# Kernel tuning notes

Hardware: AMD Instinct MI355X
Metric: run time of the kernel (lower is better)

## Reference

```python
import jax, jax.numpy as jnp
import numpy as np

T, D = 4096, 1536          # tokens, hidden
H, KV, HD = 24, 8, 64      # heads, kv heads, head dim
E, TOPK, F = 32, 8, 512    # experts, top-k, expert intermediate
FS = 1024                  # shared-MLP intermediate
THETA = 10000.0
AMULT = 0.015625           # attention_multiplier (replaces 1/sqrt(hd))
RMULT = 0.22               # residual_multiplier
EPS = 1e-6


def setup_inputs() -> dict:
    key = jax.random.key(0)
    ks = jax.random.split(key, 12)
    s = 0.02
    return {
        'positions': jnp.arange(T, dtype=jnp.int32),
        'hidden_states': jax.random.normal(ks[0], (T, D), jnp.float32),
        'ln1_w': jnp.ones((D,), jnp.float32),
        'wq': jax.random.normal(ks[1], (D, H * HD), jnp.float32) * s,
        'wk': jax.random.normal(ks[2], (D, KV * HD), jnp.float32) * s,
        'wv': jax.random.normal(ks[3], (D, KV * HD), jnp.float32) * s,
        'wo': jax.random.normal(ks[4], (H * HD, D), jnp.float32) * s,
        'ln2_w': jnp.ones((D,), jnp.float32),
        'router_w': jax.random.normal(ks[5], (D, E), jnp.float32) * s,
        'w_gate_up': jax.random.normal(ks[6], (E, D, 2 * F), jnp.float32) * s,
        'w_down': jax.random.normal(ks[7], (E, F, D), jnp.float32) * s,
        'shared_gate_up': jax.random.normal(ks[8], (D, 2 * FS), jnp.float32) * s,
        'shared_down': jax.random.normal(ks[9], (FS, D), jnp.float32) * s,
    }


def _rmsnorm(x, w):
    var = jnp.mean(x * x, axis=-1, keepdims=True)
    return x * jax.lax.rsqrt(var + EPS) * w


def _rope(x, positions):
    # x: [T, nH, HD], neox-style half rotation
    half = HD // 2
    inv_freq = 1.0 / (THETA ** (jnp.arange(half, dtype=jnp.float32) / half))
    ang = positions.astype(jnp.float32)[:, None] * inv_freq[None, :]  # [T, half]
    cos, sin = jnp.cos(ang)[:, None, :], jnp.sin(ang)[:, None, :]
    x1, x2 = x[..., :half], x[..., half:]
    return jnp.concatenate([x1 * cos - x2 * sin, x2 * cos + x1 * sin], axis=-1)


def _silu_and_mul(gu):
    g, u = jnp.split(gu, 2, axis=-1)
    return jax.nn.silu(g) * u


def reference(positions, hidden_states, ln1_w, wq, wk, wv, wo, ln2_w,
              router_w, w_gate_up, w_down, shared_gate_up, shared_down):
    # ---- attention block ----
    residual = hidden_states
    h = _rmsnorm(hidden_states, ln1_w)
    q = _rope((h @ wq).reshape(T, H, HD), positions)
    k = _rope((h @ wk).reshape(T, KV, HD), positions)
    v = (h @ wv).reshape(T, KV, HD)
    k = jnp.repeat(k, H // KV, axis=1)  # GQA expand -> [T, H, HD]
    v = jnp.repeat(v, H // KV, axis=1)
    scores = jnp.einsum('thd,shd->hts', q, k) * AMULT
    mask = jnp.tril(jnp.ones((T, T), dtype=bool))
    scores = jnp.where(mask[None], scores, jnp.finfo(scores.dtype).min)
    probs = jax.nn.softmax(scores, axis=-1)
    attn = jnp.einsum('hts,shd->thd', probs, v).reshape(T, H * HD) @ wo
    hidden = residual + attn * RMULT

    # ---- MoE + shared MLP block ----
    residual = hidden
    h = _rmsnorm(hidden, ln2_w)
    # router: top-k logits, softmax over selected (renormalized gates)
    logits = h @ router_w                          # [T, E]
    topv, topi = jax.lax.top_k(logits, TOPK)       # [T, TOPK]
    gates = jax.nn.softmax(topv, axis=-1)
    # per-token dense expert weight map [T, E] (zero for unselected experts)
    wmap = jnp.sum(jax.nn.one_hot(topi, E, dtype=h.dtype) * gates[..., None], axis=1)
    gu = jnp.einsum('td,edf->tef', h, w_gate_up)   # [T, E, 2F]
    act = _silu_and_mul(gu)                        # [T, E, F]
    moe_out = jnp.einsum('tef,efd,te->td', act, w_down, wmap)
    # shared SiLU MLP
    shared = _silu_and_mul(h @ shared_gate_up) @ shared_down
    hidden = residual + (moe_out + shared) * RMULT
    return hidden
```

## Files before the change

kernel.cpp:

```cpp
#include <hip/hip_runtime.h>
#include <stdint.h>

using u16 = unsigned short;
using u32 = unsigned int;

typedef __attribute__((ext_vector_type(8))) short short8;
typedef __attribute__((ext_vector_type(4))) short short4v;
typedef __attribute__((ext_vector_type(4))) float f32x4;

#define MFMA16(a,b,c) __builtin_amdgcn_mfma_f32_16x16x32_bf16(a,b,c,0,0,0)
#define QSCL 0.022542110325192448f


__device__ __forceinline__ u16 f2bf(float f){
  u32 u = __float_as_uint(f);
  u += 0x7fffu + ((u>>16)&1u);
  return (u16)(u>>16);
}
__device__ __forceinline__ float bf2f(u16 b){ return __uint_as_float(((u32)b)<<16); }

__device__ __forceinline__ void gload16(const void* g, void* l){
  __builtin_amdgcn_global_load_lds(
      (const __attribute__((address_space(1))) u32*)g,
      (__attribute__((address_space(3))) u32*)l, 16, 0, 0);
}

template<int CTRL>
__device__ __forceinline__ float dppf(float x){
  return __int_as_float(__builtin_amdgcn_mov_dpp(__float_as_int(x), CTRL, 0xf, 0xf, true));
}
__device__ __forceinline__ float red16_sum(float x){
  x += dppf<0x128>(x);
  x += dppf<0x124>(x);
  x += dppf<0x122>(x);
  x += dppf<0x121>(x);
  return x;
}

__global__ __launch_bounds__(256) void k_wt(const float* __restrict__ src,
    u16* __restrict__ dst, int K, int N, long sstride, long dstride)
{
  __shared__ float tile[64][65];
  int nb = blockIdx.x*64, kb = blockIdx.y*64;
  const float* S = src + (long)blockIdx.z*sstride;
  u16* D = dst + (long)blockIdx.z*dstride;
  int tid = threadIdx.x;
  int rr = tid>>4, c4 = (tid&15)*4;
  #pragma unroll
  for (int p=0;p<4;++p){
    int r = p*16 + rr;
    f32x4 v = *(const f32x4*)&S[(long)(kb+r)*N + nb + c4];
    tile[r][c4+0]=v[0]; tile[r][c4+1]=v[1]; tile[r][c4+2]=v[2]; tile[r][c4+3]=v[3];
  }
  __syncthreads();
  #pragma unroll
  for (int p=0;p<4;++p){
    int nn = p*16 + rr;
    short4v o;
    #pragma unroll
    for (int i=0;i<4;++i) o[i] = (short)f2bf(tile[c4+i][nn]);
    *(short4v*)&D[(long)(nb+nn)*K + kb + c4] = o;
  }
}

__global__ __launch_bounds__(256) void k_wti(const float* __restrict__ src,
    u16* __restrict__ dst, int K, int N, int halfN, long sstride, long dstride)
{
  __shared__ float tile[64][65];
  int nb = blockIdx.x*64, kb = blockIdx.y*64;
  const float* S = src + (long)blockIdx.z*sstride;
  u16* D = dst + (long)blockIdx.z*dstride;
  int tid = threadIdx.x;
  int rr = tid>>4, c4 = (tid&15)*4;
  int scol = (nb>>1) + ((c4>>5)<<4) + (c4&15) + (((c4>>4)&1)? halfN : 0);
  #pragma unroll
  for (int p=0;p<4;++p){
    int r = p*16 + rr;
    f32x4 v = *(const f32x4*)&S[(long)(kb+r)*N + scol];
    tile[r][c4+0]=v[0]; tile[r][c4+1]=v[1]; tile[r][c4+2]=v[2]; tile[r][c4+3]=v[3];
  }
  __syncthreads();
  #pragma unroll
  for (int p=0;p<4;++p){
    int nn = p*16 + rr;
    short4v o;
    #pragma unroll
    for (int i=0;i<4;++i) o[i] = (short)f2bf(tile[c4+i][nn]);
    *(short4v*)&D[(long)(nb+nn)*K + kb + c4] = o;
  }
}

__global__ __launch_bounds__(256) void k_vt(const u16* __restrict__ v,
                                            u16* __restrict__ vT)
{
  __shared__ u16 t_[64*72];
  int t0 = blockIdx.x*64, kvh = blockIdx.y;
  int tid = threadIdx.x;
  #pragma unroll
  for (int i=0;i<2;++i){
    int c = tid + i*256;
    int row = c>>3, dc = (c&7)*8;
    *(short8*)&t_[row*72 + dc] = *(const short8*)&v[(long)(t0+row)*2560 + kvh*64 + dc];
  }
  __syncthreads();
  #pragma unroll
  for (int i=0;i<2;++i){
    int c = tid + i*256;
    int d = c>>3, tc = (c&7)*8;
    short8 o;
    #pragma unroll
    for (int j=0;j<8;++j) o[j] = (short)t_[(tc+j)*72 + d];
    *(short8*)&vT[(long)(kvh*64 + d)*4096 + t0 + tc] = o;
  }
}

__global__ __launch_bounds__(192) void k_rmsnorm(const float* __restrict__ x,
                                                 const float* __restrict__ w,
                                                 u16* __restrict__ o)
{
  int t = blockIdx.x, tid = threadIdx.x;
  const float* xr = x + (size_t)t*1536 + tid*8;
  f32x4 a = *(const f32x4*)xr;
  f32x4 b = *(const f32x4*)(xr+4);
  float ss = a[0]*a[0]+a[1]*a[1]+a[2]*a[2]+a[3]*a[3]
           + b[0]*b[0]+b[1]*b[1]+b[2]*b[2]+b[3]*b[3];
  #pragma unroll
  for (int m=1;m<64;m<<=1) ss += __shfl_xor(ss,m);
  __shared__ float red[3];
  if ((tid&63)==0) red[tid>>6]=ss;
  __syncthreads();
  float inv = rsqrtf((red[0]+red[1]+red[2])*(1.0f/1536.0f)+1e-6f);
  const float* wp = w + tid*8;
  f32x4 wa = *(const f32x4*)wp;
  f32x4 wb = *(const f32x4*)(wp+4);
  u16* op = o + (size_t)t*1536 + tid*8;
  #pragma unroll
  for (int j=0;j<4;++j) op[j]   = f2bf(a[j]*inv*wa[j]);
  #pragma unroll
  for (int j=0;j<4;++j) op[j+4] = f2bf(b[j]*inv*wb[j]);
}

template<int MODE, int GATHER, int SWZN=0>
__global__ __launch_bounds__(256, (MODE==5||MODE==6)?4:3) void k_gemm(
    const u16* __restrict__ A, int lda,
    const u16* __restrict__ Bt, long strideB, int K,
    int Mfix, const int* __restrict__ cnts, const int* __restrict__ offs,
    const int* __restrict__ toks, const float* __restrict__ gates,
    u16* __restrict__ Cb, int ldcb,
    float* __restrict__ Cf, int ldcf,
    const float* __restrict__ resid, const int* __restrict__ pos)
{
  int e, bx, by;
  if constexpr(SWZN > 0){
    int t = blockIdx.x;
    int elo = t & 7;
    int u = t >> 3;
    int per = SWZN*32;
    int chunk = u / per;
    int inner = u - chunk*per;
    e  = elo + 8*chunk;
    bx = inner % SWZN;
    by = inner / SWZN;
  } else {
    e = blockIdx.z; bx = blockIdx.x; by = blockIdx.y;
  }
  int M = cnts ? cnts[e] : Mfix;
  int m0 = by*128;
  if (m0 >= M) return;
  int roff = offs ? offs[e] : 0;
  const u16* Bp = Bt + (long)e*strideB;
  int col0 = bx*128;

  __shared__ u16 Ash[128*64];
  __shared__ u16 Bsh[128*64];

  int tid = threadIdx.x, wv = tid>>6, lane = tid&63;
  int lr = lane&15, lg = lane>>4;
  int wr = (wv>>1)*64, wc = (wv&1)*64;

  int rsub = lane>>3;
  int ksw = ((lane&7) ^ rsub)*8;
  const u16* apt[4];
  const u16* bpt[4];
  #pragma unroll
  for (int p=0;p<4;++p){
    int rloc = p*32 + wv*8 + rsub;
    int gr = min(m0 + rloc, M-1);
    int ar = GATHER ? toks[roff + gr] : (roff + gr);
    apt[p] = A + (long)ar*lda + ksw;
    bpt[p] = Bp + (long)(col0 + rloc)*K + ksw;
  }

  f32x4 acc[4][4];
  #pragma unroll
  for (int m=0;m<4;++m)
    #pragma unroll
    for (int n=0;n<4;++n)
      acc[m][n] = (f32x4){0.f,0.f,0.f,0.f};

  int nk = K>>6;
  for (int kt=0; kt<nk; ++kt){
    __syncthreads();
    #pragma unroll
    for (int p=0;p<4;++p){
      gload16(apt[p], &Ash[(p*32 + wv*8)*64]);
      gload16(bpt[p], &Bsh[(p*32 + wv*8)*64]);
      apt[p] += 64; bpt[p] += 64;
    }
    __syncthreads();

    #pragma unroll
    for (int kk=0;kk<2;++kk){
      short8 af[4], b1[4];
      #pragma unroll
      for (int m=0;m<4;++m)
        af[m] = *(const short8*)&Ash[(wr+m*16+lr)*64 + (((kk*4+lg)^(lr&7))*8)];
      #pragma unroll
      for (int n=0;n<4;++n)
        b1[n] = *(const short8*)&Bsh[(wc+n*16+lr)*64 + (((kk*4+lg)^(lr&7))*8)];
      #pragma unroll
      for (int m=0;m<4;++m)
        #pragma unroll
        for (int n=0;n<4;++n)
          acc[m][n] = MFMA16(af[m], b1[n], acc[m][n]);
    }
  }

  if constexpr(MODE==6){
    #pragma unroll
    for (int m=0;m<4;++m)
      #pragma unroll
      for (int np=0;np<2;++np)
        #pragma unroll
        for (int rr=0;rr<4;++rr){
          int row = wr + m*16 + lg*4 + rr;
          int gr = m0 + row;
          if (gr >= M) continue;
          float g = acc[m][2*np][rr];
          float u = acc[m][2*np+1][rr];
          float s = g/(1.f+__expf(-g))*u;
          int j = (wc>>1) + np*16 + lr;
          Cb[(long)(roff+gr)*ldcb + (col0>>1) + j] = f2bf(s);
        }
  } else if constexpr(MODE==7){
    if (col0 < 2048){
      float invf0 = __expf(-(float)lr      * 0.28782313662425574f);
      float invf1 = __expf(-(float)(lr+16) * 0.28782313662425574f);
      float qs = (col0 < 1536) ? QSCL : 1.0f;
      #pragma unroll
      for (int m=0;m<4;++m)
        #pragma unroll
        for (int rr=0;rr<4;++rr){
          int gr = m0 + wr + m*16 + lg*4 + rr;
          float pv = (float)pos[gr];
          #pragma unroll
          for (int n=0;n<2;++n){
            float sn, cs;
            __sincosf(pv * (n ? invf1 : invf0), &sn, &cs);
            float x1 = acc[m][n][rr], x2 = acc[m][n+2][rr];
            long base = (long)gr*ldcb + col0 + wc + n*16 + lr;
            Cb[base]      = f2bf((x1*cs - x2*sn)*qs);
            Cb[base + 32] = f2bf((x2*cs + x1*sn)*qs);
          }
        }
    } else {
      #pragma unroll
      for (int m=0;m<4;++m)
        #pragma unroll
        for (int n=0;n<4;++n)
          #pragma unroll
          for (int rr=0;rr<4;++rr){
            int gr = m0 + wr + m*16 + lg*4 + rr;
            int col = wc + n*16 + lr;
            Cb[(long)gr*ldcb + col0 + col] = f2bf(acc[m][n][rr]);
          }
    }
  } else {
    #pragma unroll
    for (int m=0;m<4;++m)
      #pragma unroll
      for (int n=0;n<4;++n)
        #pragma unroll
        for (int rr=0;rr<4;++rr){
          int row = wr + m*16 + lg*4 + rr;
          int gr = m0 + row;
          if (gr >= M) continue;
          int col = wc + n*16 + lr;
          float va = acc[m][n][rr];
          if constexpr(MODE==0){
            Cb[(long)(roff+gr)*ldcb + col0 + col] = f2bf(va);
          } else if constexpr(MODE==1){
            long idx = (long)gr*ldcf + col0 + col;
            Cf[idx] = resid[idx] + va*0.22f;
          } else if constexpr(MODE==5){
            float gt = gates[roff+gr];
            Cb[(long)(roff+gr)*ldcb + col0 + col] = f2bf(va*gt);
          }
        }
  }
}

__global__ __launch_bounds__(192) void k_moesum(const u16* __restrict__ part,
    const int* __restrict__ inv, float* __restrict__ out)
{
  int t = blockIdx.x, tid = threadIdx.x;
  int c = tid*8;
  float s[8] = {0.f,0.f,0.f,0.f,0.f,0.f,0.f,0.f};
  #pragma unroll
  for (int kk=0;kk<8;++kk){
    int slot = inv[t*8+kk];
    short8 v = *(const short8*)&part[(long)slot*1536 + c];
    #pragma unroll
    for (int j=0;j<8;++j) s[j] += bf2f((u16)v[j]);
  }
  float* op = out + (long)t*1536 + c;
  f32x4 o0 = *(const f32x4*)op;
  f32x4 o1 = *(const f32x4*)(op+4);
  #pragma unroll
  for (int j=0;j<4;++j){ o0[j] += s[j]; o1[j] += s[j+4]; }
  *(f32x4*)op = o0;
  *(f32x4*)(op+4) = o1;
}

__global__ __launch_bounds__(256,3) void k_attn(const u16* __restrict__ qg,
    const u16* __restrict__ kg, const u16* __restrict__ vT,
    u16* __restrict__ og, u16* __restrict__ Opart, float* __restrict__ mlb)
{
  int bid = blockIdx.x;
  int kvh = bid & 7;
  int ii = bid >> 3;
  int qt, kt0, kt1, chunk; bool single;
  if (ii < 32)      { qt = 32+ii;        chunk = 0; kt0 = 0;  kt1 = 32;   single = false; }
  else if (ii < 64) { qt = ii;           chunk = 1; kt0 = 32; kt1 = qt+1; single = false; }
  else              { qt = 31-(ii-64);   chunk = 0; kt0 = 0;  kt1 = qt+1; single = true;  }

  int tid = threadIdx.x, wv = tid>>6, lane = tid&63;
  int lr = lane&15, lg = lane>>4;
  __shared__ u16 Ksh[64*72];
  __shared__ u16 Vsh[64*72];
  __shared__ u16 Psh[4][16*72];
  int q0 = qt*64;
  int qrow = q0 + wv*16 + lr;
  short8 qf[3][2];
  #pragma unroll
  for (int hh=0;hh<3;++hh)
    #pragma unroll
    for (int c=0;c<2;++c)
      qf[hh][c] = *(const short8*)&qg[(long)qrow*2560 + (kvh*3+hh)*64 + c*32 + lg*8];

  float l_[3][4];
  f32x4 Ot[3][4];
  #pragma unroll
  for (int hh=0;hh<3;++hh)
    #pragma unroll
    for (int r=0;r<4;++r) l_[hh][r]=0.f;
  #pragma unroll
  for (int hh=0;hh<3;++hh)
    #pragma unroll
    for (int d=0;d<4;++d) Ot[hh][d]=(f32x4){0.f,0.f,0.f,0.f};

  int srow = tid>>3, sdc = (tid&7)*8;
  short8 kreg[2], vreg[2];
  auto loadKV = [&](int kt){
    #pragma unroll
    for (int i=0;i<2;++i){
      int row = srow + i*32;
      kreg[i] = *(const short8*)&kg[(long)(kt*64+row)*2560 + kvh*64 + sdc];
      vreg[i] = *(const short8*)&vT[(long)(kvh*64 + row)*4096 + kt*64 + sdc];
    }
  };
  loadKV(kt0);

  for (int kt=kt0; kt<kt1; ++kt){
    __syncthreads();
    #pragma unroll
    for (int i=0;i<2;++i){
      int row = srow + i*32;
      *(short8*)&Ksh[row*72 + sdc] = kreg[i];
      *(short8*)&Vsh[row*72 + sdc] = vreg[i];
    }
    __syncthreads();
    if (kt < kt1-1) loadKV(kt+1);
    bool diag = (kt==qt);

    #pragma unroll
    for (int hh=0;hh<3;++hh){
      f32x4 S[4];
      #pragma unroll
      for (int n=0;n<4;++n) S[n]=(f32x4){0.f,0.f,0.f,0.f};
      #pragma unroll
      for (int n=0;n<4;++n)
        #pragma unroll
        for (int c=0;c<2;++c){
          short8 kf = *(const short8*)&Ksh[(n*16+lr)*72 + c*32 + lg*8];
          S[n] = MFMA16(qf[hh][c], kf, S[n]);
        }

      float rsum[4] = {0.f,0.f,0.f,0.f};
      #pragma unroll
      for (int n=0;n<4;++n)
        #pragma unroll
        for (int r=0;r<4;++r){
          float sv = S[n][r];
          if (diag){
            int colg = n*16 + lr;
            int rowg = wv*16 + lg*4 + r;
            if (colg > rowg) sv = -1e30f;
          }
          float pv = exp2f(sv);
          S[n][r] = pv;
          rsum[r] += pv;
        }
      #pragma unroll
      for (int r=0;r<4;++r) rsum[r] = red16_sum(rsum[r]);
      #pragma unroll
      for (int r=0;r<4;++r) l_[hh][r] += rsum[r];

      #pragma unroll
      for (int n=0;n<4;++n)
        #pragma unroll
        for (int r=0;r<4;++r)
          Psh[wv][(lg*4+r)*72 + n*16 + lr] = f2bf(S[n][r]);
      #pragma unroll
      for (int c=0;c<2;++c){
        short8 pf = *(const short8*)&Psh[wv][lr*72 + c*32 + lg*8];
        #pragma unroll
        for (int d=0;d<4;++d){
          short8 vf = *(const short8*)&Vsh[(d*16+lr)*72 + c*32 + lg*8];
          Ot[hh][d] = MFMA16(pf, vf, Ot[hh][d]);
        }
      }
    }
  }

  if (single){
    #pragma unroll
    for (int hh=0;hh<3;++hh)
      #pragma unroll
      for (int d=0;d<4;++d)
        #pragma unroll
        for (int r=0;r<4;++r){
          int t = q0 + wv*16 + lg*4 + r;
          og[(long)t*1536 + (kvh*3+hh)*64 + d*16 + lr] = f2bf(Ot[hh][d][r]/l_[hh][r]);
        }
  } else {
    #pragma unroll
    for (int hh=0;hh<3;++hh){
      int h = kvh*3+hh;
      #pragma unroll
      for (int r=0;r<4;++r){
        int t = q0 + wv*16 + lg*4 + r;
        long slot = ((long)(t-2048)*24 + h)*2 + chunk;
        #pragma unroll
        for (int d=0;d<4;++d)
          Opart[slot*64 + d*16 + lr] = f2bf(Ot[hh][d][r]);
        if (lr==0) mlb[slot] = l_[hh][r];
      }
    }
  }
}

__global__ __launch_bounds__(256) void k_comb(const u16* __restrict__ Opart,
    const float* __restrict__ mlb, u16* __restrict__ og)
{
  int gid = blockIdx.x*256 + threadIdx.x;
  int d = gid & 63;
  long rowi = gid >> 6;
  long s0 = rowi*2, s1 = s0+1;
  float l0 = mlb[s0], l1 = mlb[s1];
  float o = (bf2f(Opart[s0*64+d]) + bf2f(Opart[s1*64+d])) / (l0 + l1);
  int t = 2048 + (int)(rowi/24), h = (int)(rowi - (rowi/24)*24);
  og[(long)t*1536 + h*64 + d] = f2bf(o);
}

__global__ __launch_bounds__(256) void k_router(const u16* __restrict__ h2,
    const float* __restrict__ rw, int* __restrict__ topi, float* __restrict__ gatev)
{
  int t = blockIdx.x, tid = threadIdx.x;
  int e = tid & 31, seg = tid >> 5;
  const u16* hr = h2 + (size_t)t*1536 + seg*192;
  const float* wp = rw + (long)seg*192*32 + e;
  float s = 0.f;
  #pragma unroll 4
  for (int d=0; d<192; ++d)
    s += bf2f(hr[d]) * wp[(long)d*32];
  __shared__ float red[8][32];
  red[seg][e] = s;
  __syncthreads();
  __shared__ float lgt[32];
  if (tid < 32){
    float a = 0.f;
    #pragma unroll
    for (int g=0; g<8; ++g) a += red[g][tid];
    lgt[tid] = a;
  }
  __syncthreads();
  if (tid==0){
    u32 msk=0; float tv[8]; int ti[8];
    for (int kk=0;kk<8;++kk){
      float best=-1e30f; int bi=0;
      for (int j2=0;j2<32;++j2)
        if (!((msk>>j2)&1u) && lgt[j2] > best){ best=lgt[j2]; bi=j2; }
      msk |= 1u<<bi; tv[kk]=best; ti[kk]=bi;
    }
    float mx = tv[0], ssum = 0.f, ge[8];
    for (int kk=0;kk<8;++kk){ ge[kk]=__expf(tv[kk]-mx); ssum+=ge[kk]; }
    float isum = 1.f/ssum;
    for (int kk=0;kk<8;++kk){ topi[t*8+kk]=ti[kk]; gatev[t*8+kk]=ge[kk]*isum; }
  }
}

__global__ void k_hist(const int* __restrict__ topi, int* __restrict__ cnt){
  int i = blockIdx.x*256 + threadIdx.x;
  if (i < 4096*8) atomicAdd(&cnt[topi[i]], 1);
}
__global__ void k_scan(const int* __restrict__ cnt, int* __restrict__ offs, int* __restrict__ cur){
  if (threadIdx.x==0 && blockIdx.x==0){
    int a=0;
    for (int e2=0;e2<32;++e2){ offs[e2]=a; cur[e2]=a; a+=cnt[e2]; }
  }
}
__global__ void k_scatter(const int* __restrict__ topi, const float* __restrict__ gatev,
    int* __restrict__ cur, int* __restrict__ toks, float* __restrict__ gts,
    int* __restrict__ inv){
  int i = blockIdx.x*256 + threadIdx.x;
  if (i < 4096*8){
    int e2 = topi[i];
    int p = atomicAdd(&cur[e2], 1);
    toks[p] = i>>3;
    gts[p] = gatev[i]*0.22f;
    inv[i] = p;
  }
}

extern "C" void kernel_launch(void* const* d_in, const int* in_sizes, int n_in,
                              void* d_out, int out_size, void* d_ws, size_t ws_size,
                              hipStream_t stream)
{
  const int*   positions = (const int*)  d_in[0];
  const float* hs   = (const float*)d_in[1];
  const float* ln1w = (const float*)d_in[2];
  const float* wq   = (const float*)d_in[3];
  const float* wk   = (const float*)d_in[4];
  const float* wv   = (const float*)d_in[5];
  const float* wo   = (const float*)d_in[6];
  const float* ln2w = (const float*)d_in[7];
  const float* rww  = (const float*)d_in[8];
  const float* wgu  = (const float*)d_in[9];
  const float* wdn  = (const float*)d_in[10];
  const float* sgu  = (const float*)d_in[11];
  const float* sdn  = (const float*)d_in[12];
  float* out = (float*)d_out;

  char* ws = (char*)d_ws;
  size_t off = 0;
  auto alloc = [&](size_t b)->void*{ void* p = ws + off; off += (b + 255) & ~(size_t)255; return p; };

  u16* hbf     = (u16*)alloc((size_t)4096*1536*2);
  u16* qkv     = (u16*)alloc((size_t)33554432);
  u16* qkvb = qkv;
  u16* aout = qkv + (size_t)4096*2560;
  u16* act_moe = qkv;
  u16* act_sh  = (u16*)alloc((size_t)4096*1024*2);
  u16* vT      = (u16*)alloc((size_t)8*64*4096*2);
  int*   topi  = (int*)  alloc(4096*8*4);
  float* gatev = (float*)alloc(4096*8*4);
  int*   toks  = (int*)  alloc(4096*8*4);
  float* gts   = (float*)alloc(4096*8*4);
  int*   inv   = (int*)  alloc(4096*8*4);
  int*   cnt   = (int*)  alloc(512);
  int*   offs  = (int*)  alloc(512);
  int*   cur   = (int*)  alloc(512);
  u16* wqkvT = (u16*)alloc((size_t)2560*1536*2);
  u16* woT  = (u16*)alloc((size_t)1536*1536*2);
  u16* sguT = (u16*)alloc((size_t)2048*1536*2);
  u16* sdnT = (u16*)alloc((size_t)1536*1024*2);
  u16* wguT = (u16*)alloc((size_t)32*1024*1536*2);
  u16* wdnT = (u16*)alloc((size_t)32*1536*512*2);
  float* hidden2 = out;
  u16*   h2bf = hbf;
  u16*   Opart = hbf;
  float* mlb   = (float*)act_sh;
  u16*   part  = wguT;

  k_wt <<<dim3(24,24,1), 256,0,stream>>>(wq,  wqkvT,                   1536,1536, 0,0);
  k_wt <<<dim3(8,24,1),  256,0,stream>>>(wk,  wqkvT+(size_t)1536*1536, 1536,512,  0,0);
  k_wt <<<dim3(8,24,1),  256,0,stream>>>(wv,  wqkvT+(size_t)2048*1536, 1536,512,  0,0);
  k_wt <<<dim3(24,24,1), 256,0,stream>>>(wo,  woT,  1536,1536, 0,0);
  k_wti<<<dim3(32,24,1), 256,0,stream>>>(sgu, sguT, 1536,2048,1024, 0,0);
  k_wt <<<dim3(24,16,1), 256,0,stream>>>(sdn, sdnT, 1024,1536, 0,0);
  k_wti<<<dim3(16,24,32),256,0,stream>>>(wgu, wguT, 1536,1024,512, (long)1536*1024, (long)1536*1024);
  k_wt <<<dim3(24,8,32), 256,0,stream>>>(wdn, wdnT, 512,1536,  (long)512*1536,  (long)512*1536);

  k_rmsnorm<<<4096,192,0,stream>>>(hs, ln1w, hbf);
  k_gemm<7,0><<<dim3(20,32,1),256,0,stream>>>(hbf,1536, wqkvT,0,1536, 4096,nullptr,nullptr,nullptr,nullptr, qkvb,2560, nullptr,0, nullptr, positions);
  k_vt<<<dim3(64,8,1),256,0,stream>>>(qkvb + 2048, vT);
  k_attn<<<dim3(768,1,1),256,0,stream>>>(qkvb, qkvb + 1536, vT, aout, Opart, mlb);
  k_comb<<<12288,256,0,stream>>>(Opart, mlb, aout);
  k_gemm<1,0><<<dim3(12,32,1),256,0,stream>>>(aout,1536, woT,0,1536, 4096,nullptr,nullptr,nullptr,nullptr, nullptr,0, hidden2,1536, hs, nullptr);
  k_rmsnorm<<<4096,192,0,stream>>>(hidden2, ln2w, h2bf);
  k_router<<<4096,256,0,stream>>>(h2bf, rww, topi, gatev);
  hipMemsetAsync(cnt, 0, 32*4, stream);
  k_hist<<<128,256,0,stream>>>(topi, cnt);
  k_scan<<<1,64,0,stream>>>(cnt, offs, cur);
  k_scatter<<<128,256,0,stream>>>(topi, gatev, cur, toks, gts, inv);
  k_gemm<6,1,8><<<dim3(8192,1,1),256,0,stream>>>(h2bf,1536, wguT,(long)1024*1536,1536, 0,cnt,offs,toks,nullptr, act_moe,512, nullptr,0, nullptr, nullptr);
  k_gemm<6,0><<<dim3(16,32,1),256,0,stream>>>(h2bf,1536, sguT,0,1536, 4096,nullptr,nullptr,nullptr,nullptr, act_sh,1024, nullptr,0, nullptr, nullptr);
  k_gemm<1,0><<<dim3(12,32,1),256,0,stream>>>(act_sh,1024, sdnT,0,1024, 4096,nullptr,nullptr,nullptr,nullptr, nullptr,0, out,1536, out, nullptr);
  k_gemm<5,0,12><<<dim3(12288,1,1),256,0,stream>>>(act_moe,512, wdnT,(long)1536*512,512, 0,cnt,offs,nullptr,gts, part,1536, nullptr,0, nullptr, nullptr);
  k_moesum<<<4096,192,0,stream>>>(part, inv, out);

  (void)in_sizes; (void)n_in; (void)out_size; (void)ws_size;
}
```

Before: 863.1 us.

## Split causal attention into 16-tile KV chunks for finer load balance

Reworks the attention work split. Each query tile's KV range is now cut into chunks of at most 16 tiles, giving 160 chunk slots per kv head and 1280 blocks. Previously only the upper half of the query tiles was split into two chunks. Every chunk writes unnormalized partials and row sums to a new dedicated workspace buffer, and the combine kernel sums 1 to 4 chunks for all tokens. It also raises the occupancy hint to 4 blocks per CU and shrinks the P scratch pitch, at the cost of more partial traffic and a combine pass over the whole sequence.

```diff
diff --git a/kernel.cpp b/kernel.cpp
--- a/kernel.cpp
+++ b/kernel.cpp
@@ -322,31 +322,33 @@
   *(f32x4*)(op+4) = o1;
 }
 
-__global__ __launch_bounds__(256,3) void k_attn(const u16* __restrict__ qg,
+__global__ __launch_bounds__(256,4) void k_attn(const u16* __restrict__ qg,
     const u16* __restrict__ kg, const u16* __restrict__ vT,
-    u16* __restrict__ og, u16* __restrict__ Opart, float* __restrict__ mlb)
+    u16* __restrict__ Opart, float* __restrict__ lsum)
 {
   int bid = blockIdx.x;
   int kvh = bid & 7;
-  int ii = bid >> 3;
-  int qt, kt0, kt1, chunk; bool single;
-  if (ii < 32)      { qt = 32+ii;        chunk = 0; kt0 = 0;  kt1 = 32;   single = false; }
-  else if (ii < 64) { qt = ii;           chunk = 1; kt0 = 32; kt1 = qt+1; single = false; }
-  else              { qt = 31-(ii-64);   chunk = 0; kt0 = 0;  kt1 = qt+1; single = true;  }
+  int s = 159 - (bid >> 3);
+  int qt, c;
+  if (s < 16)      { qt = s;               c = 0; }
+  else if (s < 48) { int d2 = s-16; qt = 16 + (d2>>1); c = d2&1; }
+  else if (s < 96) { int d2 = s-48; qt = 32 + d2/3;    c = d2%3; }
+  else             { int d2 = s-96; qt = 48 + (d2>>2); c = d2&3; }
+  int kt0 = c*16, kt1 = min(kt0+16, qt+1);
 
   int tid = threadIdx.x, wv = tid>>6, lane = tid&63;
   int lr = lane&15, lg = lane>>4;
   __shared__ u16 Ksh[64*72];
   __shared__ u16 Vsh[64*72];
-  __shared__ u16 Psh[4][16*72];
+  __shared__ u16 Psh[4][16*68];
   int q0 = qt*64;
   int qrow = q0 + wv*16 + lr;
   short8 qf[3][2];
   #pragma unroll
   for (int hh=0;hh<3;++hh)
     #pragma unroll
-    for (int c=0;c<2;++c)
-      qf[hh][c] = *(const short8*)&qg[(long)qrow*2560 + (kvh*3+hh)*64 + c*32 + lg*8];
+    for (int cc=0;cc<2;++cc)
+      qf[hh][cc] = *(const short8*)&qg[(long)qrow*2560 + (kvh*3+hh)*64 + cc*32 + lg*8];
 
   float l_[3][4];
   f32x4 Ot[3][4];
@@ -391,9 +393,9 @@
       #pragma unroll
       for (int n=0;n<4;++n)
         #pragma unroll
-        for (int c=0;c<2;++c){
-          short8 kf = *(const short8*)&Ksh[(n*16+lr)*72 + c*32 + lg*8];
-          S[n] = MFMA16(qf[hh][c], kf, S[n]);
+        for (int cc=0;cc<2;++cc){
+          short8 kf = *(const short8*)&Ksh[(n*16+lr)*72 + cc*32 + lg*8];
+          S[n] = MFMA16(qf[hh][cc], kf, S[n]);
         }
 
       float rsum[4] = {0.f,0.f,0.f,0.f};
@@ -420,57 +422,53 @@
       for (int n=0;n<4;++n)
         #pragma unroll
         for (int r=0;r<4;++r)
-          Psh[wv][(lg*4+r)*72 + n*16 + lr] = f2bf(S[n][r]);
-      #pragma unroll
-      for (int c=0;c<2;++c){
-        short8 pf = *(const short8*)&Psh[wv][lr*72 + c*32 + lg*8];
+          Psh[wv][(lg*4+r)*68 + n*16 + lr] = f2bf(S[n][r]);
+      #pragma unroll
+      for (int cc=0;cc<2;++cc){
+        short8 pf = *(const short8*)&Psh[wv][lr*68 + cc*32 + lg*8];
         #pragma unroll
         for (int d=0;d<4;++d){
-          short8 vf = *(const short8*)&Vsh[(d*16+lr)*72 + c*32 + lg*8];
+          short8 vf = *(const short8*)&Vsh[(d*16+lr)*72 + cc*32 + lg*8];
           Ot[hh][d] = MFMA16(pf, vf, Ot[hh][d]);
         }
       }
     }
   }
 
-  if (single){
-    #pragma unroll
-    for (int hh=0;hh<3;++hh)
+  #pragma unroll
+  for (int hh=0;hh<3;++hh){
+    int h = kvh*3+hh;
+    #pragma unroll
+    for (int r=0;r<4;++r){
+      int u = wv*16 + lg*4 + r;
+      long slot = ((long)(s*64 + u))*24 + h;
       #pragma unroll
       for (int d=0;d<4;++d)
-        #pragma unroll
-        for (int r=0;r<4;++r){
-          int t = q0 + wv*16 + lg*4 + r;
-          og[(long)t*1536 + (kvh*3+hh)*64 + d*16 + lr] = f2bf(Ot[hh][d][r]/l_[hh][r]);
-        }
-  } else {
-    #pragma unroll
-    for (int hh=0;hh<3;++hh){
-      int h = kvh*3+hh;
-      #pragma unroll
-      for (int r=0;r<4;++r){
-        int t = q0 + wv*16 + lg*4 + r;
-        long slot = ((long)(t-2048)*24 + h)*2 + chunk;
-        #pragma unroll
-        for (int d=0;d<4;++d)
-          Opart[slot*64 + d*16 + lr] = f2bf(Ot[hh][d][r]);
-        if (lr==0) mlb[slot] = l_[hh][r];
-      }
+        Opart[slot*64 + d*16 + lr] = f2bf(Ot[hh][d][r]);
+      if (lr==0) lsum[slot] = l_[hh][r];
     }
   }
 }
 
 __global__ __launch_bounds__(256) void k_comb(const u16* __restrict__ Opart,
-    const float* __restrict__ mlb, u16* __restrict__ og)
+    const float* __restrict__ lsum, u16* __restrict__ og)
 {
   int gid = blockIdx.x*256 + threadIdx.x;
   int d = gid & 63;
-  long rowi = gid >> 6;
-  long s0 = rowi*2, s1 = s0+1;
-  float l0 = mlb[s0], l1 = mlb[s1];
-  float o = (bf2f(Opart[s0*64+d]) + bf2f(Opart[s1*64+d])) / (l0 + l1);
-  int t = 2048 + (int)(rowi/24), h = (int)(rowi - (rowi/24)*24);
-  og[(long)t*1536 + h*64 + d] = f2bf(o);
+  int rowi = gid >> 6;
+  int t = rowi/24, h = rowi - t*24;
+  int qt = t>>6;
+  int g = qt>>4;
+  int nc = g+1;
+  int sB = 16*((g*(g+1))>>1) + (qt&15)*nc;
+  int u = t & 63;
+  float osum = 0.f, ls = 0.f;
+  for (int c=0; c<nc; ++c){
+    long slot = ((long)((sB+c)*64 + u))*24 + h;
+    osum += bf2f(Opart[slot*64 + d]);
+    ls   += lsum[slot];
+  }
+  og[(long)t*1536 + h*64 + d] = f2bf(osum/ls);
 }
 
 __global__ __launch_bounds__(256) void k_router(const u16* __restrict__ h2,
@@ -563,6 +561,8 @@
   u16* act_moe = qkv;
   u16* act_sh  = (u16*)alloc((size_t)4096*1024*2);
   u16* vT      = (u16*)alloc((size_t)8*64*4096*2);
+  u16* Opart   = (u16*)alloc((size_t)160*64*24*64*2);
+  float* lsum  = (float*)alloc((size_t)160*64*24*4);
   int*   topi  = (int*)  alloc(4096*8*4);
   float* gatev = (float*)alloc(4096*8*4);
   int*   toks  = (int*)  alloc(4096*8*4);
@@ -579,8 +579,6 @@
   u16* wdnT = (u16*)alloc((size_t)32*1536*512*2);
   float* hidden2 = out;
   u16*   h2bf = hbf;
-  u16*   Opart = hbf;
-  float* mlb   = (float*)act_sh;
   u16*   part  = wguT;
 
   k_wt <<<dim3(24,24,1), 256,0,stream>>>(wq,  wqkvT,                   1536,1536, 0,0);
@@ -595,8 +593,8 @@
   k_rmsnorm<<<4096,192,0,stream>>>(hs, ln1w, hbf);
   k_gemm<7,0><<<dim3(20,32,1),256,0,stream>>>(hbf,1536, wqkvT,0,1536, 4096,nullptr,nullptr,nullptr,nullptr, qkvb,2560, nullptr,0, nullptr, positions);
   k_vt<<<dim3(64,8,1),256,0,stream>>>(qkvb + 2048, vT);
-  k_attn<<<dim3(768,1,1),256,0,stream>>>(qkvb, qkvb + 1536, vT, aout, Opart, mlb);
-  k_comb<<<12288,256,0,stream>>>(Opart, mlb, aout);
+  k_attn<<<dim3(1280,1,1),256,0,stream>>>(qkvb, qkvb + 1536, vT, Opart, lsum);
+  k_comb<<<24576,256,0,stream>>>(Opart, lsum, aout);
   k_gemm<1,0><<<dim3(12,32,1),256,0,stream>>>(aout,1536, woT,0,1536, 4096,nullptr,nullptr,nullptr,nullptr, nullptr,0, hidden2,1536, hs, nullptr);
   k_rmsnorm<<<4096,192,0,stream>>>(hidden2, ln2w, h2bf);
   k_router<<<4096,256,0,stream>>>(h2bf, rww, topi, gatev);
```

Result: slower. 927.2 us (+7.4%).
